# Optimization experiments

Measured on AMD Instinct MI355X. Metric: run time of the kernel, lower is better.

The kernel has to match this reference:

```python
import jax, jax.numpy as jnp
import numpy as np

B, N, M = 2, 2048, 8192
C1, C = 256, 128
K, SHARE = 16, 8
BN_EPS = 1e-5


def bn(x, g, b):
    # eval-mode BatchNorm1d with running_mean=0, running_var=1
    return x * (g / jnp.sqrt(1.0 + BN_EPS)) + b


def setup_inputs() -> dict:
    key = jax.random.key(0)
    ks = iter(jax.random.split(key, 64))
    nrm = lambda shape, s=0.05: jax.random.normal(next(ks), shape, dtype=jnp.float32) * s
    ones = lambda n: jnp.ones((n,), jnp.float32)
    zeros = lambda n: jnp.zeros((n,), jnp.float32)
    CS = C // SHARE  # 16
    return {
        # forward args
        "xyz": jax.random.uniform(next(ks), (B, N, 3), dtype=jnp.float32),
        "feature": jax.random.normal(next(ks), (B, C1, N), dtype=jnp.float32),
        "target_xyz": jax.random.uniform(next(ks), (B, M, 3), dtype=jnp.float32),
        "target_feature": jax.random.normal(next(ks), (B, C, M), dtype=jnp.float32),
        # TransitionUp (is_head=False): two Conv1d(k=1, bias=False)+BN+ReLU
        "tu_lin1_w": nrm((C, C1)), "tu_bn1_g": ones(C), "tu_bn1_b": zeros(C),
        "tu_lin2_w": nrm((C, C)), "tu_bn2_g": ones(C), "tu_bn2_b": zeros(C),
        # PointTransformerBlock(128,128, share_planes=8, nsample=16)
        "blk_lin1_w": nrm((C, C)), "blk_bn1_g": ones(C), "blk_bn1_b": zeros(C),
        "wq": nrm((C, C)), "bq": zeros(C),
        "wk": nrm((C, C)), "bk": zeros(C),
        "wv": nrm((C, C)), "bv": zeros(C),
        # position MLP: Linear(3,3)+BN+ReLU+Linear(3,C)
        "p1_w": nrm((3, 3), 0.3), "p1_b": zeros(3), "p_bn_g": ones(3), "p_bn_b": zeros(3),
        "p2_w": nrm((C, 3), 0.3), "p2_b": zeros(C),
        # attention weight MLP: BN(C)+ReLU+Linear(C,CS)+BN(CS)+ReLU+Linear(CS,CS)
        "w_bn1_g": ones(C), "w_bn1_b": zeros(C),
        "w_lin1_w": nrm((CS, C)), "w_lin1_b": zeros(CS),
        "w_bn2_g": ones(CS), "w_bn2_b": zeros(CS),
        "w_lin2_w": nrm((CS, CS)), "w_lin2_b": zeros(CS),
        "blk_bn2_g": ones(C), "blk_bn2_b": zeros(C),
        "blk_lin3_w": nrm((C, C)), "blk_bn3_g": ones(C), "blk_bn3_b": zeros(C),
    }


def reference(xyz, feature, target_xyz, target_feature,
              tu_lin1_w, tu_bn1_g, tu_bn1_b, tu_lin2_w, tu_bn2_g, tu_bn2_b,
              blk_lin1_w, blk_bn1_g, blk_bn1_b,
              wq, bq, wk, bk, wv, bv,
              p1_w, p1_b, p_bn_g, p_bn_b, p2_w, p2_b,
              w_bn1_g, w_bn1_b, w_lin1_w, w_lin1_b, w_bn2_g, w_bn2_b, w_lin2_w, w_lin2_b,
              blk_bn2_g, blk_bn2_b, blk_lin3_w, blk_bn3_g, blk_bn3_b):
    # ---------------- TransitionUp (feature upsampling N -> M) ----------------
    # three_nn: 3 nearest source points for each target point
    d2 = jnp.sum((target_xyz[:, :, None, :] - xyz[:, None, :, :]) ** 2, -1)  # [B,M,N]
    negd, idx3 = jax.lax.top_k(-d2, 3)                                       # [B,M,3]
    dist = jnp.sqrt(jnp.maximum(-negd, 0.0))
    rec = 1.0 / (dist + 1e-8)
    weight = rec / jnp.sum(rec, -1, keepdims=True)                           # [B,M,3]

    f = jnp.einsum('oc,bcn->bon', tu_lin1_w, feature)                        # [B,C,N]
    f = jax.nn.relu(bn(f, tu_bn1_g[None, :, None], tu_bn1_b[None, :, None]))

    # three_interpolate: weighted gather of 3-NN features
    gath = jax.vmap(lambda fb, ib: fb[:, ib])(f, idx3)                       # [B,C,M,3]
    interp = jnp.sum(gath * weight[:, None, :, :], -1)                       # [B,C,M]

    tf = jnp.einsum('oc,bcm->bom', tu_lin2_w, target_feature)
    tf = jax.nn.relu(bn(tf, tu_bn2_g[None, :, None], tu_bn2_b[None, :, None]))
    feat = tf + interp                                                        # [B,C,M]

    # ---------------- PointTransformerBlock (local kNN vector attention) ----------------
    x = feat.transpose(0, 2, 1)                                               # [B,M,C]
    identity = x
    x1 = jax.nn.relu(bn(x @ blk_lin1_w.T, blk_bn1_g, blk_bn1_b))              # [B,M,C]

    # kNN among target points (includes self, distance 0)
    d2t = jnp.sum((target_xyz[:, :, None, :] - target_xyz[:, None, :, :]) ** 2, -1)  # [B,M,M]
    _, knn = jax.lax.top_k(-d2t, K)                                           # [B,M,K]

    q = x1 @ wq.T + bq
    k = x1 @ wk.T + bk
    v = x1 @ wv.T + bv
    gather_nb = jax.vmap(lambda tb, ib: tb[ib])                               # [M,C],[M,K] -> [M,K,C]
    xk = gather_nb(k, knn)                                                    # [B,M,K,C]
    xv = gather_nb(v, knn)                                                    # [B,M,K,C]

    # relative positional encoding
    pr = gather_nb(target_xyz, knn) - target_xyz[:, :, None, :]               # [B,M,K,3]
    pr = jax.nn.relu(bn(pr @ p1_w.T + p1_b, p_bn_g, p_bn_b)) @ p2_w.T + p2_b  # [B,M,K,C]

    r = xk - q[:, :, None, :] + pr                                            # [B,M,K,C]
    w = jax.nn.relu(bn(r, w_bn1_g, w_bn1_b)) @ w_lin1_w.T + w_lin1_b          # [B,M,K,CS]
    w = jax.nn.relu(bn(w, w_bn2_g, w_bn2_b)) @ w_lin2_w.T + w_lin2_b          # [B,M,K,CS]
    w = jax.nn.softmax(w, axis=2)                                             # over K neighbors

    CS = C // SHARE
    agg = jnp.sum((xv + pr).reshape(B, M, K, SHARE, CS) * w[:, :, :, None, :], axis=2)
    agg = agg.reshape(B, M, C)

    x2 = jax.nn.relu(bn(agg, blk_bn2_g, blk_bn2_b))
    x3 = bn(x2 @ blk_lin3_w.T, blk_bn3_g, blk_bn3_b)
    out = jax.nn.relu(x3 + identity)                                          # [B,M,C]
    return out.transpose(0, 2, 1)                                             # [B,C,M]
```

## Files before the change

kernel.cpp:

```cpp
#include <hip/hip_runtime.h>
#include <cstddef>
#include <cstdint>

#define B_  2
#define N_  2048
#define M_  8192
#define C1_ 256
#define C_  128
#define K_  16
#define CS_ 16

#define BNINV 0.9999950000374997f

#define LDSA 17
#define LDSB 33

__device__ __forceinline__ void stage_direct64(float4* Ls4, const float4* src4,
                                               size_t row_stride4, int k0,
                                               size_t col0_4, int t)
{
#pragma unroll
    for (int i = 0; i < 2; ++i) {
        int idx = t + i * 256;
        int kk = idx >> 4, f4 = idx & 15;
        Ls4[kk * LDSA + f4] = src4[(size_t)(k0 + kk) * row_stride4 + col0_4 + f4];
    }
}

__device__ __forceinline__ void stage_transposeA(float* Lsf, const float* src,
                                                 int row0, int ldk, int k0, int t)
{
    int u = t & 7, r = t >> 3;
#pragma unroll
    for (int i = 0; i < 2; ++i) {
        int row = r + i * 32;
        float4 v = *(const float4*)(src + (size_t)(row0 + row) * ldk + k0 + u * 4);
        Lsf[(u * 4 + 0) * 68 + row] = v.x;
        Lsf[(u * 4 + 1) * 68 + row] = v.y;
        Lsf[(u * 4 + 2) * 68 + row] = v.z;
        Lsf[(u * 4 + 3) * 68 + row] = v.w;
    }
}

__device__ __forceinline__ void stage_transposeB(float* Lsf, const float* src,
                                                 int ldk, int k0, int t)
{
    int u = t & 7, r = t >> 3;
#pragma unroll
    for (int i = 0; i < 4; ++i) {
        int row = r + i * 32;
        float4 v = *(const float4*)(src + (size_t)row * ldk + k0 + u * 4);
        Lsf[(u * 4 + 0) * 132 + row] = v.x;
        Lsf[(u * 4 + 1) * 132 + row] = v.y;
        Lsf[(u * 4 + 2) * 132 + row] = v.z;
        Lsf[(u * 4 + 3) * 132 + row] = v.w;
    }
}

__device__ __forceinline__ void gemm_step64(const float4* As4, const float4* Bs4,
                                            int tm, int tn, float acc[4][8])
{
#pragma unroll 4
    for (int kk = 0; kk < 32; ++kk) {
        float4 a0 = As4[kk * LDSA + tm];
        float4 b0 = Bs4[kk * LDSB + tn * 2];
        float4 b1 = Bs4[kk * LDSB + tn * 2 + 1];
        float av[4] = {a0.x,a0.y,a0.z,a0.w};
        float bv[8] = {b0.x,b0.y,b0.z,b0.w,b1.x,b1.y,b1.z,b1.w};
#pragma unroll
        for (int i = 0; i < 4; ++i)
#pragma unroll
            for (int j = 0; j < 8; ++j)
                acc[i][j] = fmaf(av[i], bv[j], acc[i][j]);
    }
}

__device__ __forceinline__ void load8(const float* p, float* v)
{
    float4 a = *(const float4*)p, b = *(const float4*)(p + 4);
    v[0]=a.x; v[1]=a.y; v[2]=a.z; v[3]=a.w; v[4]=b.x; v[5]=b.y; v[6]=b.z; v[7]=b.w;
}
__device__ __forceinline__ void store8(float* p, const float* v)
{
    *(float4*)p       = make_float4(v[0],v[1],v[2],v[3]);
    *(float4*)(p + 4) = make_float4(v[4],v[5],v[6],v[7]);
}

extern "C" __global__ __launch_bounds__(256) void k_f(
    const float* __restrict__ feature, const float* __restrict__ w,
    const float* __restrict__ g, const float* __restrict__ bb,
    float* __restrict__ f_t)
{
    __shared__ float4 As4[32 * LDSA], Bs4[32 * LDSB];
    int t = threadIdx.x, tm = t >> 4, tn = t & 15;
    int m0 = blockIdx.x * 64;
    int b = m0 >> 11;
    size_t col0_4 = (size_t)(m0 & (N_ - 1)) >> 2;
    const float4* src4 = (const float4*)feature + (size_t)b * C1_ * (N_ / 4);
    float acc[4][8] = {};
    for (int k0 = 0; k0 < C1_; k0 += 32) {
        stage_direct64(As4, src4, N_ / 4, k0, col0_4, t);
        stage_transposeB((float*)Bs4, w, C1_, k0, t);
        __syncthreads();
        gemm_step64(As4, Bs4, tm, tn, acc);
        __syncthreads();
    }
    int c0 = tn * 8;
    float gc[8], bc[8];
    load8(g + c0, gc); load8(bb + c0, bc);
#pragma unroll
    for (int mm = 0; mm < 4; ++mm) {
        int m = m0 + tm * 4 + mm;
        float o[8];
#pragma unroll
        for (int j = 0; j < 8; ++j)
            o[j] = fmaxf(fmaf(acc[mm][j], gc[j] * BNINV, bc[j]), 0.f);
        store8(f_t + (size_t)m * C_ + c0, o);
    }
}

extern "C" __global__ __launch_bounds__(256) void k_soa(
    const float* __restrict__ txyz,
    float* __restrict__ cx, float* __restrict__ cy, float* __restrict__ cz)
{
    int t = blockIdx.x * 256 + threadIdx.x;
    if (t < B_ * M_) {
        cx[t] = txyz[t*3+0];
        cy[t] = txyz[t*3+1];
        cz[t] = txyz[t*3+2];
    }
}

extern "C" __global__ __launch_bounds__(256) void k_three_nn(
    const float* __restrict__ xyz, const float* __restrict__ txyz,
    int* __restrict__ idx3, float* __restrict__ w3)
{
    int q    = blockIdx.x * 4 + (threadIdx.x >> 6);
    int lane = threadIdx.x & 63;
    int b    = q / M_;
    const float* src = xyz + (size_t)b * N_ * 3;
    float qx = txyz[(size_t)q*3+0], qy = txyz[(size_t)q*3+1], qz = txyz[(size_t)q*3+2];

    unsigned long long p0 = ~0ULL, p1 = ~0ULL, p2 = ~0ULL;
    for (int i = 0; i < N_/64; ++i) {
        int j = lane + (i << 6);
        float dx = src[j*3+0]-qx, dy = src[j*3+1]-qy, dz = src[j*3+2]-qz;
        float d = __fadd_rn(__fadd_rn(__fmul_rn(dx,dx), __fmul_rn(dy,dy)), __fmul_rn(dz,dz));
        unsigned long long key = ((unsigned long long)__float_as_uint(d) << 32) | (unsigned)j;
        if (key < p2) {
            p2 = key;
            if (p2 < p1) { unsigned long long t = p1; p1 = p2; p2 = t; }
            if (p1 < p0) { unsigned long long t = p0; p0 = p1; p1 = t; }
        }
    }
    unsigned long long wmin[3];
    unsigned long long h = p0;
#pragma unroll
    for (int r = 0; r < 3; ++r) {
        unsigned long long w = h;
#pragma unroll
        for (int s = 1; s < 64; s <<= 1) {
            unsigned long long o = __shfl_xor(w, s, 64);
            w = (o < w) ? o : w;
        }
        wmin[r] = w;
        if (h == w) { p0 = p1; p1 = p2; p2 = ~0ULL; h = p0; }
    }
    if (lane == 0) {
        float d0 = __uint_as_float((unsigned)(wmin[0] >> 32));
        float d1 = __uint_as_float((unsigned)(wmin[1] >> 32));
        float d2 = __uint_as_float((unsigned)(wmin[2] >> 32));
        float s0 = sqrtf(fmaxf(d0, 0.f)), s1 = sqrtf(fmaxf(d1, 0.f)), s2 = sqrtf(fmaxf(d2, 0.f));
        float r0 = 1.f/(s0+1e-8f), r1 = 1.f/(s1+1e-8f), r2 = 1.f/(s2+1e-8f);
        float inv = 1.f/(r0+r1+r2);
        idx3[(size_t)q*3+0] = (int)(unsigned)wmin[0];
        idx3[(size_t)q*3+1] = (int)(unsigned)wmin[1];
        idx3[(size_t)q*3+2] = (int)(unsigned)wmin[2];
        w3[(size_t)q*3+0] = r0*inv; w3[(size_t)q*3+1] = r1*inv; w3[(size_t)q*3+2] = r2*inv;
    }
}

extern "C" __global__ __launch_bounds__(256) void k_feat(
    const float* __restrict__ tfeat, const float* __restrict__ w2,
    const float* __restrict__ g, const float* __restrict__ bb,
    const float* __restrict__ f_t, const int* __restrict__ idx3,
    const float* __restrict__ w3, float* __restrict__ x)
{
    __shared__ float4 As4[32 * LDSA], Bs4[32 * LDSB];
    int t = threadIdx.x, tm = t >> 4, tn = t & 15;
    int m0 = blockIdx.x * 64;
    int b = m0 >> 13;
    size_t col0_4 = (size_t)(m0 & (M_ - 1)) >> 2;
    const float4* src4 = (const float4*)tfeat + (size_t)b * C_ * (M_ / 4);
    float acc[4][8] = {};
    for (int k0 = 0; k0 < C_; k0 += 32) {
        stage_direct64(As4, src4, M_ / 4, k0, col0_4, t);
        stage_transposeB((float*)Bs4, w2, C_, k0, t);
        __syncthreads();
        gemm_step64(As4, Bs4, tm, tn, acc);
        __syncthreads();
    }
    int c0 = tn * 8;
    float gc[8], bc[8];
    load8(g + c0, gc); load8(bb + c0, bc);
    const float* fb = f_t + (size_t)b * N_ * C_;
#pragma unroll
    for (int mm = 0; mm < 4; ++mm) {
        int m = m0 + tm * 4 + mm;
        int   i0 = idx3[m*3+0], i1 = idx3[m*3+1], i2 = idx3[m*3+2];
        float u0 = w3[m*3+0],  u1 = w3[m*3+1],  u2 = w3[m*3+2];
        float r0[8], r1[8], r2[8];
        load8(fb + (size_t)i0 * C_ + c0, r0);
        load8(fb + (size_t)i1 * C_ + c0, r1);
        load8(fb + (size_t)i2 * C_ + c0, r2);
        float o[8];
#pragma unroll
        for (int j = 0; j < 8; ++j) {
            float y = fmaxf(fmaf(acc[mm][j], gc[j] * BNINV, bc[j]), 0.f);
            o[j] = y + u0 * r0[j] + u1 * r1[j] + u2 * r2[j];
        }
        store8(x + (size_t)m * C_ + c0, o);
    }
}

extern "C" __global__ __launch_bounds__(256) void k_knn(
    const float* __restrict__ cx, const float* __restrict__ cy,
    const float* __restrict__ cz, int* __restrict__ out_knn)
{
    int q    = blockIdx.x * 4 + (threadIdx.x >> 6);
    int lane = threadIdx.x & 63;
    int b    = q >> 13;
    const float4* bx4 = (const float4*)(cx + (size_t)b * M_);
    const float4* by4 = (const float4*)(cy + (size_t)b * M_);
    const float4* bz4 = (const float4*)(cz + (size_t)b * M_);
    float qx = cx[q], qy = cy[q], qz = cz[q];

    unsigned long long list = ~0ULL;
    unsigned long long tau  = ~0ULL;
    float taud = 3e38f;

#define DIST(px,py,pz) ({ \
    float dx = (px)-qx, dy = (py)-qy, dz = (pz)-qz; \
    __fadd_rn(__fadd_rn(__fmul_rn(dx,dx), __fmul_rn(dy,dy)), __fmul_rn(dz,dz)); })

#define MIN4 (min(min(k0,k1),min(k2,k3)))

#define MERGELOOP { \
    unsigned long long mask = __ballot(mk < tau); \
    while (mask) { \
        int srcl = (int)__ffsll((long long)mask) - 1; \
        unsigned long long kk = __shfl(mk, srcl, 64); \
        unsigned long long below = __ballot(list < kk) & 0xFFFFull; \
        int pos = __popcll(below); \
        unsigned long long sh = __shfl_up(list, 1, 64); \
        if (lane == pos)                  list = kk; \
        else if (lane > pos && lane < K_) list = sh; \
        tau = __shfl(list, K_ - 1, 64); \
        if (lane == srcl) { \
            if      (k0 == mk) k0 = ~0ULL; \
            else if (k1 == mk) k1 = ~0ULL; \
            else if (k2 == mk) k2 = ~0ULL; \
            else               k3 = ~0ULL; \
            mk = MIN4; \
        } \
        mask = __ballot(mk < tau); \
    } \
    taud = __uint_as_float((unsigned)(tau >> 32)); }

    {
        float4 px = bx4[lane], py = by4[lane], pz = bz4[lane];
        float d0 = DIST(px.x,py.x,pz.x);
        float d1 = DIST(px.y,py.y,pz.y);
        float d2 = DIST(px.z,py.z,pz.z);
        float d3 = DIST(px.w,py.w,pz.w);
        unsigned long long j0 = (unsigned)(lane*4);
        unsigned long long k0 = ((unsigned long long)__float_as_uint(d0) << 32) | (j0+0);
        unsigned long long k1 = ((unsigned long long)__float_as_uint(d1) << 32) | (j0+1);
        unsigned long long k2 = ((unsigned long long)__float_as_uint(d2) << 32) | (j0+2);
        unsigned long long k3 = ((unsigned long long)__float_as_uint(d3) << 32) | (j0+3);
        unsigned long long key = k0;
#pragma unroll
        for (int k = 2; k <= 64; k <<= 1) {
#pragma unroll
            for (int j = k >> 1; j > 0; j >>= 1) {
                unsigned long long o = __shfl_xor(key, j, 64);
                bool up  = ((lane & k) == 0);
                bool low = ((lane & j) == 0);
                bool keepmin = (low == up);
                unsigned long long mn = (o < key) ? o : key;
                unsigned long long mx = (o < key) ? key : o;
                key = keepmin ? mn : mx;
            }
        }
        if (lane < K_) list = key;
        tau  = __shfl(list, K_ - 1, 64);
        taud = __uint_as_float((unsigned)(tau >> 32));
        k0 = ~0ULL;
        unsigned long long mk = MIN4;
        MERGELOOP
    }

    for (int i = 1; i < M_/256; ++i) {
        float4 px = bx4[i*64 + lane];
        float4 py = by4[i*64 + lane];
        float4 pz = bz4[i*64 + lane];
        float d0 = DIST(px.x,py.x,pz.x);
        float d1 = DIST(px.y,py.y,pz.y);
        float d2 = DIST(px.z,py.z,pz.z);
        float d3 = DIST(px.w,py.w,pz.w);
        bool any = (d0 <= taud) | (d1 <= taud) | (d2 <= taud) | (d3 <= taud);
        if (__ballot(any)) {
            unsigned long long j0 = (unsigned)(i*256 + lane*4);
            unsigned long long k0 = ((unsigned long long)__float_as_uint(d0) << 32) | (j0+0);
            unsigned long long k1 = ((unsigned long long)__float_as_uint(d1) << 32) | (j0+1);
            unsigned long long k2 = ((unsigned long long)__float_as_uint(d2) << 32) | (j0+2);
            unsigned long long k3 = ((unsigned long long)__float_as_uint(d3) << 32) | (j0+3);
            unsigned long long mk = MIN4;
            MERGELOOP
        }
    }
#undef MERGELOOP
#undef MIN4
#undef DIST
    if (lane < K_)
        out_knn[(size_t)q*K_ + lane] = (int)(unsigned)list;
}

extern "C" __global__ __launch_bounds__(256) void k_lin(
    const float* __restrict__ xin, const float* __restrict__ w,
    const float* __restrict__ g, const float* __restrict__ bb,
    float* __restrict__ xout)
{
    __shared__ float4 As4[32 * LDSA], Bs4[32 * LDSB];
    int t = threadIdx.x, tm = t >> 4, tn = t & 15;
    int m0 = blockIdx.x * 64;
    float acc[4][8] = {};
    for (int k0 = 0; k0 < C_; k0 += 32) {
        stage_transposeA((float*)As4, xin, m0, C_, k0, t);
        stage_transposeB((float*)Bs4, w, C_, k0, t);
        __syncthreads();
        gemm_step64(As4, Bs4, tm, tn, acc);
        __syncthreads();
    }
    int c0 = tn * 8;
    float gc[8], bc[8];
    load8(g + c0, gc); load8(bb + c0, bc);
#pragma unroll
    for (int mm = 0; mm < 4; ++mm) {
        int m = m0 + tm * 4 + mm;
        float o[8];
#pragma unroll
        for (int j = 0; j < 8; ++j)
            o[j] = fmaxf(fmaf(acc[mm][j], gc[j] * BNINV, bc[j]), 0.f);
        store8(xout + (size_t)m * C_ + c0, o);
    }
}

extern "C" __global__ __launch_bounds__(256) void k_qkv(
    const float* __restrict__ x1,
    const float* __restrict__ wq, const float* __restrict__ bq,
    const float* __restrict__ wk, const float* __restrict__ bk,
    const float* __restrict__ wv, const float* __restrict__ bv,
    float* __restrict__ q, float* __restrict__ k, float* __restrict__ v)
{
    __shared__ float4 As4[32 * LDSA], Bs4[32 * LDSB];
    int t = threadIdx.x, tm = t >> 4, tn = t & 15;
    int m0 = blockIdx.x * 64;
    int which = blockIdx.y;
    const float* W  = (which == 0) ? wq : (which == 1) ? wk : wv;
    const float* bi = (which == 0) ? bq : (which == 1) ? bk : bv;
    float*       out= (which == 0) ? q  : (which == 1) ? k  : v;
    float acc[4][8] = {};
    for (int k0 = 0; k0 < C_; k0 += 32) {
        stage_transposeA((float*)As4, x1, m0, C_, k0, t);
        stage_transposeB((float*)Bs4, W, C_, k0, t);
        __syncthreads();
        gemm_step64(As4, Bs4, tm, tn, acc);
        __syncthreads();
    }
    int c0 = tn * 8;
    float bc[8];
    load8(bi + c0, bc);
#pragma unroll
    for (int mm = 0; mm < 4; ++mm) {
        int m = m0 + tm * 4 + mm;
        float o[8];
#pragma unroll
        for (int j = 0; j < 8; ++j) o[j] = acc[mm][j] + bc[j];
        store8(out + (size_t)m * C_ + c0, o);
    }
}

extern "C" __global__ __launch_bounds__(128) void k_attn2(
    const float* __restrict__ q, const float* __restrict__ kf, const float* __restrict__ vf,
    const int* __restrict__ knn, const float* __restrict__ txyz,
    const float* __restrict__ p1w, const float* __restrict__ p1b,
    const float* __restrict__ pbg, const float* __restrict__ pbb,
    const float* __restrict__ p2w, const float* __restrict__ p2b,
    const float* __restrict__ wb1g, const float* __restrict__ wb1b,
    const float* __restrict__ wl1, const float* __restrict__ wl1b,
    const float* __restrict__ wb2g, const float* __restrict__ wb2b,
    const float* __restrict__ wl2, const float* __restrict__ wl2b,
    const float* __restrict__ bn2g, const float* __restrict__ bn2b,
    float* __restrict__ x2out)
{
    __shared__ float tshs[K_ * C_];
    __shared__ float svs [K_ * C_];
    __shared__ float wl1s[CS_ * 132];
    __shared__ float wl2s[CS_ * 17];
    __shared__ float ashs[K_ * 17];
    __shared__ float wshs[K_ * 17];

    int bm = blockIdx.x;
    int b  = bm >> 13;
    int c  = threadIdx.x;

#pragma unroll
    for (int i = 0; i < 16; ++i) {
        int idx = c + i * 128;
        wl1s[(idx >> 7) * 132 + (idx & 127)] = wl1[idx];
    }
    {
        int i1 = c, i2 = c + 128;
        if (i1 < 256) wl2s[(i1 >> 4) * 17 + (i1 & 15)] = wl2[i1];
        if (i2 < 256) wl2s[(i2 >> 4) * 17 + (i2 & 15)] = wl2[i2];
    }

    float qc = q[(size_t)bm * C_ + c];
    float qx = txyz[(size_t)bm*3+0], qy = txyz[(size_t)bm*3+1], qz = txyz[(size_t)bm*3+2];
    float p2w0 = p2w[c*3+0], p2w1 = p2w[c*3+1], p2w2 = p2w[c*3+2], p2bc = p2b[c];
    float b1s = wb1g[c]*BNINV, b1b = wb1b[c];
    float a00=p1w[0],a01=p1w[1],a02=p1w[2],a10=p1w[3],a11=p1w[4],a12=p1w[5],a20=p1w[6],a21=p1w[7],a22=p1w[8];
    float pb0=p1b[0], pb1=p1b[1], pb2=p1b[2];
    float g0=pbg[0]*BNINV, g1=pbg[1]*BNINV, g2=pbg[2]*BNINV;
    float hb0=pbb[0], hb1=pbb[1], hb2=pbb[2];
    const float* txb = txyz + (size_t)b * M_ * 3;

    __syncthreads();

    for (int t = 0; t < K_; ++t) {
        int nb = knn[(size_t)bm*K_ + t];
        float dx = txb[nb*3+0]-qx, dy = txb[nb*3+1]-qy, dz = txb[nb*3+2]-qz;
        float h0 = fmaxf(fmaf(fmaf(a02,dz, fmaf(a01,dy, fmaf(a00,dx, pb0))), g0, hb0), 0.f);
        float h1 = fmaxf(fmaf(fmaf(a12,dz, fmaf(a11,dy, fmaf(a10,dx, pb1))), g1, hb1), 0.f);
        float h2 = fmaxf(fmaf(fmaf(a22,dz, fmaf(a21,dy, fmaf(a20,dx, pb2))), g2, hb2), 0.f);
        float pr = fmaf(p2w2,h2, fmaf(p2w1,h1, fmaf(p2w0,h0, p2bc)));
        size_t nrow = ((size_t)b*M_ + nb)*C_ + c;
        float r = kf[nrow] - qc + pr;
        tshs[t*C_ + c] = fmaxf(fmaf(r, b1s, b1b), 0.f);
        svs [t*C_ + c] = vf[nrow] + pr;
    }
    __syncthreads();

    {
        int s = c >> 3, u = c & 7;
        float w1b = wl1b[s], gg = wb2g[s]*BNINV, gb = wb2b[s];
        for (int nb = 0; nb < K_; ++nb) {
            float a = 0.f;
#pragma unroll
            for (int i = 0; i < 16; ++i)
                a = fmaf(wl1s[s*132 + u + 8*i], tshs[nb*C_ + u + 8*i], a);
            a += __shfl_down(a, 4, 8);
            a += __shfl_down(a, 2, 8);
            a += __shfl_down(a, 1, 8);
            if (u == 0)
                ashs[nb*17 + s] = fmaxf(fmaf(a + w1b, gg, gb), 0.f);
        }
    }
    __syncthreads();

    {
        int nb = c >> 3;
        int cs1 = c & 7, cs2 = (c & 7) + 8;
        float a1 = wl2b[cs1], a2 = wl2b[cs2];
#pragma unroll
        for (int j = 0; j < CS_; ++j) {
            float av = ashs[nb*17 + j];
            a1 = fmaf(wl2s[cs1*17 + j], av, a1);
            a2 = fmaf(wl2s[cs2*17 + j], av, a2);
        }
        wshs[nb*17 + cs1] = a1;
        wshs[nb*17 + cs2] = a2;
    }
    __syncthreads();

    if (c < CS_) {
        float mx = -3e38f;
#pragma unroll
        for (int nb = 0; nb < K_; ++nb) mx = fmaxf(mx, wshs[nb*17 + c]);
        float ssum = 0.f;
#pragma unroll
        for (int nb = 0; nb < K_; ++nb) {
            float e = __expf(wshs[nb*17 + c] - mx);
            wshs[nb*17 + c] = e; ssum += e;
        }
        float inv = 1.f / ssum;
#pragma unroll
        for (int nb = 0; nb < K_; ++nb) wshs[nb*17 + c] *= inv;
    }
    __syncthreads();

    float agg = 0.f;
    int cs = c & (CS_ - 1);
#pragma unroll
    for (int nb = 0; nb < K_; ++nb)
        agg = fmaf(svs[nb*C_ + c], wshs[nb*17 + cs], agg);
    float x2 = fmaxf(fmaf(agg, bn2g[c]*BNINV, bn2b[c]), 0.f);
    x2out[(size_t)bm * C_ + c] = x2;
}

extern "C" __global__ __launch_bounds__(256) void k_lin3(
    const float* __restrict__ x2, const float* __restrict__ w,
    const float* __restrict__ g, const float* __restrict__ bb,
    const float* __restrict__ xid, float* __restrict__ out)
{
    __shared__ float4 As4[32 * LDSA], Bs4[32 * LDSB];
    int t = threadIdx.x, tm = t >> 4, tn = t & 15;
    int m0 = blockIdx.x * 64;
    int b  = m0 >> 13;
    float acc[4][8] = {};
    for (int k0 = 0; k0 < C_; k0 += 32) {
        stage_transposeA((float*)As4, x2, m0, C_, k0, t);
        stage_transposeB((float*)Bs4, w, C_, k0, t);
        __syncthreads();
        gemm_step64(As4, Bs4, tm, tn, acc);
        __syncthreads();
    }
    int c0 = tn * 8;
    float gc[8], bc[8];
    load8(g + c0, gc); load8(bb + c0, bc);
#pragma unroll
    for (int mm = 0; mm < 4; ++mm) {
        int m = m0 + tm * 4 + mm;
        float idv[8];
        load8(xid + (size_t)m * C_ + c0, idv);
#pragma unroll
        for (int j = 0; j < 8; ++j) {
            float x3 = fmaf(acc[mm][j], gc[j] * BNINV, bc[j]);
            acc[mm][j] = fmaxf(x3 + idv[j], 0.f);
        }
    }
    int mloc = (m0 & (M_ - 1)) + tm * 4;
    float* ob = out + (size_t)b * C_ * M_;
#pragma unroll
    for (int j = 0; j < 8; ++j) {
        float* p = ob + (size_t)(c0 + j) * M_ + mloc;
        *(float4*)p = make_float4(acc[0][j], acc[1][j], acc[2][j], acc[3][j]);
    }
}

extern "C" void kernel_launch(void* const* d_in, const int* in_sizes, int n_in,
                              void* d_out, int out_size, void* d_ws, size_t ws_size,
                              hipStream_t stream)
{
    const float* xyz   = (const float*)d_in[0];
    const float* feat  = (const float*)d_in[1];
    const float* txyz  = (const float*)d_in[2];
    const float* tfeat = (const float*)d_in[3];
    const float* tu1w  = (const float*)d_in[4];
    const float* tu1g  = (const float*)d_in[5];
    const float* tu1b  = (const float*)d_in[6];
    const float* tu2w  = (const float*)d_in[7];
    const float* tu2g  = (const float*)d_in[8];
    const float* tu2b  = (const float*)d_in[9];
    const float* bl1w  = (const float*)d_in[10];
    const float* bl1g  = (const float*)d_in[11];
    const float* bl1b  = (const float*)d_in[12];
    const float* wq    = (const float*)d_in[13];
    const float* bq    = (const float*)d_in[14];
    const float* wk    = (const float*)d_in[15];
    const float* bk    = (const float*)d_in[16];
    const float* wv    = (const float*)d_in[17];
    const float* bv    = (const float*)d_in[18];
    const float* p1w   = (const float*)d_in[19];
    const float* p1b   = (const float*)d_in[20];
    const float* pbg   = (const float*)d_in[21];
    const float* pbb   = (const float*)d_in[22];
    const float* p2w   = (const float*)d_in[23];
    const float* p2b   = (const float*)d_in[24];
    const float* wb1g  = (const float*)d_in[25];
    const float* wb1b  = (const float*)d_in[26];
    const float* wl1   = (const float*)d_in[27];
    const float* wl1b  = (const float*)d_in[28];
    const float* wb2g  = (const float*)d_in[29];
    const float* wb2b  = (const float*)d_in[30];
    const float* wl2   = (const float*)d_in[31];
    const float* wl2b  = (const float*)d_in[32];
    const float* bn2g  = (const float*)d_in[33];
    const float* bn2b  = (const float*)d_in[34];
    const float* l3w   = (const float*)d_in[35];
    const float* bn3g  = (const float*)d_in[36];
    const float* bn3b  = (const float*)d_in[37];

    char* ws = (char*)d_ws;
    size_t off = 0;
    auto alloc = [&](size_t bytes) { void* p = ws + off; off += (bytes + 255) & ~(size_t)255; return p; };
    float* f_t  = (float*)alloc(sizeof(float) * B_ * N_ * C_);
    int*   idx3 = (int*)  alloc(sizeof(int)   * B_ * M_ * 3);
    float* w3   = (float*)alloc(sizeof(float) * B_ * M_ * 3);
    float* x    = (float*)alloc(sizeof(float) * B_ * M_ * C_);
    float* x1   = (float*)alloc(sizeof(float) * B_ * M_ * C_);
    float* qb   = (float*)alloc(sizeof(float) * B_ * M_ * C_);
    float* kb   = (float*)alloc(sizeof(float) * B_ * M_ * C_);
    float* vb   = (float*)alloc(sizeof(float) * B_ * M_ * C_);
    int*   knn  = (int*)  alloc(sizeof(int)   * B_ * M_ * K_);
    float* cx   = (float*)alloc(sizeof(float) * B_ * M_);
    float* cy   = (float*)alloc(sizeof(float) * B_ * M_);
    float* cz   = (float*)alloc(sizeof(float) * B_ * M_);
    float* x2   = x1;

    k_soa     <<<(B_*M_+255)/256, 256, 0, stream>>>(txyz, cx, cy, cz);
    k_f       <<<B_*N_/64,        256, 0, stream>>>(feat, tu1w, tu1g, tu1b, f_t);
    k_three_nn<<<B_*M_/4,         256, 0, stream>>>(xyz, txyz, idx3, w3);
    k_feat    <<<B_*M_/64,        256, 0, stream>>>(tfeat, tu2w, tu2g, tu2b, f_t, idx3, w3, x);
    k_knn     <<<B_*M_/4,         256, 0, stream>>>(cx, cy, cz, knn);
    k_lin     <<<B_*M_/64,        256, 0, stream>>>(x, bl1w, bl1g, bl1b, x1);
    k_qkv     <<<dim3(B_*M_/64,3),256, 0, stream>>>(x1, wq, bq, wk, bk, wv, bv, qb, kb, vb);
    k_attn2   <<<B_*M_,           128, 0, stream>>>(qb, kb, vb, knn, txyz,
                                                    p1w, p1b, pbg, pbb, p2w, p2b,
                                                    wb1g, wb1b, wl1, wl1b, wb2g, wb2b, wl2, wl2b,
                                                    bn2g, bn2b, x2);
    k_lin3    <<<B_*M_/64,        256, 0, stream>>>(x2, l3w, bn3g, bn3b, x, (float*)d_out);
}
```

Before: 378.1 us.

## Fuse lin1 and QKV GEMMs, prefetch neighbor rows in attention kernel

Merges the block lin1 GEMM with the Q/K/V projections into one kernel that keeps the 64-row activation tile resident in LDS, avoiding the x1 round-trip to global memory and re-staging A three times. The attention kernel now loads neighbor indices and coordinates into shared memory first and issues all 16 k/v gathers up front into registers, exposing memory-level parallelism. The trade-off is a larger LDS footprint (about 34KB for the A tile), which lowers occupancy, plus a 3x serial loop per block and more register pressure in the attention kernel.

After: 374.0 us. Within noise of the previous version (-1.1%).

```diff
diff --git a/kernel.cpp b/kernel.cpp
--- a/kernel.cpp
+++ b/kernel.cpp
@@ -326,68 +326,65 @@
         out_knn[(size_t)q*K_ + lane] = (int)(unsigned)list;
 }
 
-extern "C" __global__ __launch_bounds__(256) void k_lin(
-    const float* __restrict__ xin, const float* __restrict__ w,
-    const float* __restrict__ g, const float* __restrict__ bb,
-    float* __restrict__ xout)
-{
-    __shared__ float4 As4[32 * LDSA], Bs4[32 * LDSB];
-    int t = threadIdx.x, tm = t >> 4, tn = t & 15;
-    int m0 = blockIdx.x * 64;
-    float acc[4][8] = {};
-    for (int k0 = 0; k0 < C_; k0 += 32) {
-        stage_transposeA((float*)As4, xin, m0, C_, k0, t);
-        stage_transposeB((float*)Bs4, w, C_, k0, t);
-        __syncthreads();
-        gemm_step64(As4, Bs4, tm, tn, acc);
-        __syncthreads();
-    }
-    int c0 = tn * 8;
-    float gc[8], bc[8];
-    load8(g + c0, gc); load8(bb + c0, bc);
-#pragma unroll
-    for (int mm = 0; mm < 4; ++mm) {
-        int m = m0 + tm * 4 + mm;
-        float o[8];
-#pragma unroll
-        for (int j = 0; j < 8; ++j)
-            o[j] = fmaxf(fmaf(acc[mm][j], gc[j] * BNINV, bc[j]), 0.f);
-        store8(xout + (size_t)m * C_ + c0, o);
-    }
-}
-
-extern "C" __global__ __launch_bounds__(256) void k_qkv(
-    const float* __restrict__ x1,
+extern "C" __global__ __launch_bounds__(256) void k_lqkv(
+    const float* __restrict__ xin,
+    const float* __restrict__ w1, const float* __restrict__ g1, const float* __restrict__ b1,
     const float* __restrict__ wq, const float* __restrict__ bq,
     const float* __restrict__ wk, const float* __restrict__ bk,
     const float* __restrict__ wv, const float* __restrict__ bv,
     float* __restrict__ q, float* __restrict__ k, float* __restrict__ v)
 {
-    __shared__ float4 As4[32 * LDSA], Bs4[32 * LDSB];
+    __shared__ float  Asf[128 * 68];
+    __shared__ float4 Bs4[32 * LDSB];
     int t = threadIdx.x, tm = t >> 4, tn = t & 15;
     int m0 = blockIdx.x * 64;
-    int which = blockIdx.y;
-    const float* W  = (which == 0) ? wq : (which == 1) ? wk : wv;
-    const float* bi = (which == 0) ? bq : (which == 1) ? bk : bv;
-    float*       out= (which == 0) ? q  : (which == 1) ? k  : v;
+    int c0 = tn * 8;
+
+    for (int k0 = 0; k0 < C_; k0 += 32)
+        stage_transposeA(Asf + k0 * 68, xin, m0, C_, k0, t);
+
     float acc[4][8] = {};
     for (int k0 = 0; k0 < C_; k0 += 32) {
-        stage_transposeA((float*)As4, x1, m0, C_, k0, t);
-        stage_transposeB((float*)Bs4, W, C_, k0, t);
-        __syncthreads();
-        gemm_step64(As4, Bs4, tm, tn, acc);
-        __syncthreads();
-    }
-    int c0 = tn * 8;
-    float bc[8];
-    load8(bi + c0, bc);
-#pragma unroll
-    for (int mm = 0; mm < 4; ++mm) {
-        int m = m0 + tm * 4 + mm;
-        float o[8];
-#pragma unroll
-        for (int j = 0; j < 8; ++j) o[j] = acc[mm][j] + bc[j];
-        store8(out + (size_t)m * C_ + c0, o);
+        stage_transposeB((float*)Bs4, w1, C_, k0, t);
+        __syncthreads();
+        gemm_step64((const float4*)Asf + k0 * 17, Bs4, tm, tn, acc);
+        __syncthreads();
+    }
+    {
+        float gc[8], bc[8];
+        load8(g1 + c0, gc); load8(b1 + c0, bc);
+#pragma unroll
+        for (int mm = 0; mm < 4; ++mm) {
+            int ml = tm * 4 + mm;
+#pragma unroll
+            for (int j = 0; j < 8; ++j)
+                Asf[(c0 + j) * 68 + ml] = fmaxf(fmaf(acc[mm][j], gc[j] * BNINV, bc[j]), 0.f);
+        }
+    }
+    __syncthreads();
+
+#pragma unroll 1
+    for (int which = 0; which < 3; ++which) {
+        const float* W  = (which == 0) ? wq : (which == 1) ? wk : wv;
+        const float* bi = (which == 0) ? bq : (which == 1) ? bk : bv;
+        float*       out= (which == 0) ? q  : (which == 1) ? k  : v;
+        float acc2[4][8] = {};
+        for (int k0 = 0; k0 < C_; k0 += 32) {
+            stage_transposeB((float*)Bs4, W, C_, k0, t);
+            __syncthreads();
+            gemm_step64((const float4*)Asf + k0 * 17, Bs4, tm, tn, acc2);
+            __syncthreads();
+        }
+        float bc[8];
+        load8(bi + c0, bc);
+#pragma unroll
+        for (int mm = 0; mm < 4; ++mm) {
+            int m = m0 + tm * 4 + mm;
+            float o[8];
+#pragma unroll
+            for (int j = 0; j < 8; ++j) o[j] = acc2[mm][j] + bc[j];
+            store8(out + (size_t)m * C_ + c0, o);
+        }
     }
 }
 
@@ -404,6 +401,8 @@
     const float* __restrict__ bn2g, const float* __restrict__ bn2b,
     float* __restrict__ x2out)
 {
+    __shared__ int   nbs[K_];
+    __shared__ float scrd[K_][3];
     __shared__ float tshs[K_ * C_];
     __shared__ float svs [K_ * C_];
     __shared__ float wl1s[CS_ * 132];
@@ -424,6 +423,21 @@
         int i1 = c, i2 = c + 128;
         if (i1 < 256) wl2s[(i1 >> 4) * 17 + (i1 & 15)] = wl2[i1];
         if (i2 < 256) wl2s[(i2 >> 4) * 17 + (i2 & 15)] = wl2[i2];
+    }
+    if (c < K_) nbs[c] = knn[(size_t)bm * K_ + c];
+    __syncthreads();
+
+    float kfv[K_], vfv[K_];
+    const float* txb = txyz + (size_t)b * M_ * 3;
+#pragma unroll
+    for (int t = 0; t < K_; ++t) {
+        size_t nrow = ((size_t)b * M_ + nbs[t]) * C_ + c;
+        kfv[t] = kf[nrow];
+        vfv[t] = vf[nrow];
+    }
+    if (c < 48) {
+        int t = c / 3, comp = c - t * 3;
+        scrd[t][comp] = txb[nbs[t] * 3 + comp];
     }
 
     float qc = q[(size_t)bm * C_ + c];
@@ -434,21 +448,18 @@
     float pb0=p1b[0], pb1=p1b[1], pb2=p1b[2];
     float g0=pbg[0]*BNINV, g1=pbg[1]*BNINV, g2=pbg[2]*BNINV;
     float hb0=pbb[0], hb1=pbb[1], hb2=pbb[2];
-    const float* txb = txyz + (size_t)b * M_ * 3;
-
     __syncthreads();
 
+#pragma unroll
     for (int t = 0; t < K_; ++t) {
-        int nb = knn[(size_t)bm*K_ + t];
-        float dx = txb[nb*3+0]-qx, dy = txb[nb*3+1]-qy, dz = txb[nb*3+2]-qz;
+        float dx = scrd[t][0]-qx, dy = scrd[t][1]-qy, dz = scrd[t][2]-qz;
         float h0 = fmaxf(fmaf(fmaf(a02,dz, fmaf(a01,dy, fmaf(a00,dx, pb0))), g0, hb0), 0.f);
         float h1 = fmaxf(fmaf(fmaf(a12,dz, fmaf(a11,dy, fmaf(a10,dx, pb1))), g1, hb1), 0.f);
         float h2 = fmaxf(fmaf(fmaf(a22,dz, fmaf(a21,dy, fmaf(a20,dx, pb2))), g2, hb2), 0.f);
         float pr = fmaf(p2w2,h2, fmaf(p2w1,h1, fmaf(p2w0,h0, p2bc)));
-        size_t nrow = ((size_t)b*M_ + nb)*C_ + c;
-        float r = kf[nrow] - qc + pr;
+        float r = kfv[t] - qc + pr;
         tshs[t*C_ + c] = fmaxf(fmaf(r, b1s, b1b), 0.f);
-        svs [t*C_ + c] = vf[nrow] + pr;
+        svs [t*C_ + c] = vfv[t] + pr;
     }
     __syncthreads();
 
@@ -599,7 +610,7 @@
     int*   idx3 = (int*)  alloc(sizeof(int)   * B_ * M_ * 3);
     float* w3   = (float*)alloc(sizeof(float) * B_ * M_ * 3);
     float* x    = (float*)alloc(sizeof(float) * B_ * M_ * C_);
-    float* x1   = (float*)alloc(sizeof(float) * B_ * M_ * C_);
+    float* x2   = (float*)alloc(sizeof(float) * B_ * M_ * C_);
     float* qb   = (float*)alloc(sizeof(float) * B_ * M_ * C_);
     float* kb   = (float*)alloc(sizeof(float) * B_ * M_ * C_);
     float* vb   = (float*)alloc(sizeof(float) * B_ * M_ * C_);
@@ -607,15 +618,14 @@
     float* cx   = (float*)alloc(sizeof(float) * B_ * M_);
     float* cy   = (float*)alloc(sizeof(float) * B_ * M_);
     float* cz   = (float*)alloc(sizeof(float) * B_ * M_);
-    float* x2   = x1;
 
     k_soa     <<<(B_*M_+255)/256, 256, 0, stream>>>(txyz, cx, cy, cz);
     k_f       <<<B_*N_/64,        256, 0, stream>>>(feat, tu1w, tu1g, tu1b, f_t);
     k_three_nn<<<B_*M_/4,         256, 0, stream>>>(xyz, txyz, idx3, w3);
     k_feat    <<<B_*M_/64,        256, 0, stream>>>(tfeat, tu2w, tu2g, tu2b, f_t, idx3, w3, x);
     k_knn     <<<B_*M_/4,         256, 0, stream>>>(cx, cy, cz, knn);
-    k_lin     <<<B_*M_/64,        256, 0, stream>>>(x, bl1w, bl1g, bl1b, x1);
-    k_qkv     <<<dim3(B_*M_/64,3),256, 0, stream>>>(x1, wq, bq, wk, bk, wv, bv, qb, kb, vb);
+    k_lqkv    <<<B_*M_/64,        256, 0, stream>>>(x, bl1w, bl1g, bl1b,
+                                                    wq, bq, wk, bk, wv, bv, qb, kb, vb);
     k_attn2   <<<B_*M_,           128, 0, stream>>>(qb, kb, vb, knn, txyz,
                                                     p1w, p1b, pbg, pbb, p2w, p2b,
                                                     wb1g, wb1b, wl1, wl1b, wb2g, wb2b, wl2, wl2b,
```
